# Kernel tuning notes

Hardware: AMD Instinct MI355X
Metric: run time of the kernel (lower is better)

Reference implementation:

```python
import jax, jax.numpy as jnp
import numpy as np

D_MODEL = 256

def setup_inputs() -> dict:
    key = jax.random.key(0)
    ks = jax.random.split(key, 6)
    B, Tx, Tm, D = 4, 512, 512, D_MODEL
    s = 1.0 / np.sqrt(D)
    return {
        "x": jax.random.normal(ks[0], (B, Tx, D), jnp.float32),
        "memory": jax.random.normal(ks[1], (B, Tm, D), jnp.float32),
        "memory_mask": jnp.ones((B, Tm), jnp.int32),
        "ws1_w": jax.random.uniform(ks[2], (D, D), jnp.float32, -s, s),
        "ws1_b": jax.random.uniform(ks[3], (D,), jnp.float32, -s, s),
        "ws2_w": jax.random.uniform(ks[4], (D, D), jnp.float32, -s, s),
        "wst_w": jax.random.uniform(ks[5], (D,), jnp.float32, -s, s),
    }

def reference(x, memory, memory_mask, ws1_w, ws1_b, ws2_w, wst_w):
    # item1: [B,Tx,D], item2: [B,Tm,D]  (torch Linear: y = x @ W^T + b)
    item1 = jnp.einsum("bxd,ed->bxe", x, ws1_w) + ws1_b
    item2 = jnp.einsum("bmd,ed->bme", memory, ws2_w)
    # broadcast add -> [B,Tx,Tm,D], tanh, reduce by wst -> scores [B,Tx,Tm]
    item = jnp.tanh(item1[:, :, None, :] + item2[:, None, :, :])
    S = jnp.einsum("bxmd,d->bxm", item, wst_w)
    S = jnp.where(memory_mask[:, None, :] == 0, -jnp.inf, S)
    S = jax.nn.softmax(S, axis=-1)
    out = jnp.einsum("bxm,bmd->bxd", S, memory)
    return (out, S)
```

## Files before the change

kernel.cpp:

```cpp
#include <hip/hip_runtime.h>

#define D_MODEL 256
#define TX 512
#define TM 512

__device__ __forceinline__ float fexp2(float x) { return __builtin_amdgcn_exp2f(x); }
__device__ __forceinline__ float frcp(float x)  { return __builtin_amdgcn_rcpf(x); }

__device__ __forceinline__ float quad(float4 a, float4 e, float4 w, float acc) {
    float p1 = fmaf(a.x, e.x, 1.f);
    float p2 = fmaf(a.y, e.y, 1.f);
    float p3 = fmaf(a.z, e.z, 1.f);
    float p4 = fmaf(a.w, e.w, 1.f);
    float p12 = p1 * p2;
    float p34 = p3 * p4;
    float q12 = fmaf(w.x, p2, w.y * p1);
    float q34 = fmaf(w.z, p4, w.w * p3);
    float N   = fmaf(q12, p34, q34 * p12);
    float D   = p12 * p34;
    return fmaf(N, frcp(D), acc);
}

__global__ __launch_bounds__(128) void gemm_exp2(
    const float* __restrict__ x,   const float* __restrict__ mem,
    const float* __restrict__ w1,  const float* __restrict__ b1,
    const float* __restrict__ w2,
    float* __restrict__ E1, float* __restrict__ E2p)
{
    const float C_SCALE = 2.8853900817779268f;
    const int bid = (int)blockIdx.x;
    const float* A; const float* W;
    int r0, n0;
    if (blockIdx.z == 0) { A = x;  W = w1; r0 = (bid & 63) * 32; n0 = (bid >> 6) * 64; }
    else                 { A = w2; W = mem; r0 = (bid & 7) * 32;  n0 = (bid >> 3) * 64; }

    __shared__ float As[2][16][36];
    __shared__ float Ws[2][16][68];
    const int tid = threadIdx.x;
    const int tx = tid & 15, ty = tid >> 4;
    const int rl = tid >> 2, g = tid & 3;
    float acc[4][4] = {};
    const float* Ap  = A + (size_t)(r0 + rl) * 256 + g * 4;
    const float* Wp0 = W + (size_t)(n0 + rl) * 256 + g * 4;
    const float* Wp1 = W + (size_t)(n0 + 32 + rl) * 256 + g * 4;

    {
        float4 a4 = *(const float4*)Ap;
        float4 w4 = *(const float4*)Wp0;
        float4 w5 = *(const float4*)Wp1;
        As[0][g*4+0][rl] = a4.x; As[0][g*4+1][rl] = a4.y;
        As[0][g*4+2][rl] = a4.z; As[0][g*4+3][rl] = a4.w;
        Ws[0][g*4+0][rl] = w4.x; Ws[0][g*4+1][rl] = w4.y;
        Ws[0][g*4+2][rl] = w4.z; Ws[0][g*4+3][rl] = w4.w;
        Ws[0][g*4+0][rl+32] = w5.x; Ws[0][g*4+1][rl+32] = w5.y;
        Ws[0][g*4+2][rl+32] = w5.z; Ws[0][g*4+3][rl+32] = w5.w;
    }
    __syncthreads();

    for (int k0 = 0; k0 < 16; ++k0) {
        const int cur = k0 & 1;
        float4 an, wn, vn;
        if (k0 < 15) {
            an = *(const float4*)(Ap  + (k0 + 1) * 16);
            wn = *(const float4*)(Wp0 + (k0 + 1) * 16);
            vn = *(const float4*)(Wp1 + (k0 + 1) * 16);
        }
        #pragma unroll
        for (int kk = 0; kk < 16; ++kk) {
            float4 av = *(const float4*)&As[cur][kk][ty*4];
            float4 wv = *(const float4*)&Ws[cur][kk][tx*4];
            float a_[4] = {av.x, av.y, av.z, av.w};
            float w_[4] = {wv.x, wv.y, wv.z, wv.w};
            #pragma unroll
            for (int i = 0; i < 4; ++i)
                #pragma unroll
                for (int j = 0; j < 4; ++j)
                    acc[i][j] = fmaf(a_[i], w_[j], acc[i][j]);
        }
        if (k0 < 15) {
            const int nxt = cur ^ 1;
            As[nxt][g*4+0][rl] = an.x; As[nxt][g*4+1][rl] = an.y;
            As[nxt][g*4+2][rl] = an.z; As[nxt][g*4+3][rl] = an.w;
            Ws[nxt][g*4+0][rl] = wn.x; Ws[nxt][g*4+1][rl] = wn.y;
            Ws[nxt][g*4+2][rl] = wn.z; Ws[nxt][g*4+3][rl] = wn.w;
            Ws[nxt][g*4+0][rl+32] = vn.x; Ws[nxt][g*4+1][rl+32] = vn.y;
            Ws[nxt][g*4+2][rl+32] = vn.z; Ws[nxt][g*4+3][rl+32] = vn.w;
            __syncthreads();
        }
    }

    if (blockIdx.z == 0) {
        #pragma unroll
        for (int i = 0; i < 4; ++i) {
            const int r = r0 + ty*4 + i;
            #pragma unroll
            for (int j = 0; j < 4; ++j) {
                const int n = n0 + tx*4 + j;
                E1[(size_t)r*256 + n] = fexp2(C_SCALE * (acc[i][j] + b1[n]));
            }
        }
    } else {
        #pragma unroll
        for (int i = 0; i < 4; ++i) {
            const int r = r0 + ty*4 + i;
            #pragma unroll
            for (int j = 0; j < 4; ++j) {
                const int n = n0 + tx*4 + j;
                E2p[(size_t)(r >> 2)*8192 + (size_t)n*4 + (r & 3)] = fexp2(C_SCALE * acc[i][j]);
            }
        }
    }
}

__global__ __launch_bounds__(512) void fused_tanh_attn(
    const float* __restrict__ E1,
    const float* __restrict__ E2p,
    const float* __restrict__ memory,
    const int*   __restrict__ mask,
    const float* __restrict__ wst,
    float* __restrict__ out,
    float* __restrict__ Sout)
{
    const float LOG2E = 1.4426950408889634f;
    const int t = threadIdx.x;
    const int blk = (int)((blockIdx.x & 7) * 64 + (blockIdx.x >> 3));
    const int b = blk >> 7;
    const int x0 = (blk & 127) * 4;
    const int wave = t >> 6, lane = t & 63;
    const int tm = t & 255;
    const int dh = t >> 8;

    __shared__ float i1R[4][D_MODEL];
    __shared__ float wsh[D_MODEL];
    __shared__ float P[4][TM];
    __shared__ float mneg[TM];
    __shared__ float opart[8][4][D_MODEL];
    __shared__ float wpart[8];
    __shared__ float smax[4][2], ssum[4][2];

    {
        const float* i1g = E1 + ((size_t)b * TX + x0) * D_MODEL;
        const int row = t >> 7, col2 = (t & 127) * 2;
        float2 v = *(const float2*)(i1g + (size_t)row * D_MODEL + col2);
        *(float2*)&i1R[row][col2] = v;
    }
    if (t < 256) wsh[t] = wst[t];
    mneg[t] = mask[b*TM + t] ? 0.f : -__builtin_inff();

    {
        float s = (t < 256) ? wst[t] : 0.f;
        #pragma unroll
        for (int off = 32; off > 0; off >>= 1) s += __shfl_xor(s, off);
        if (lane == 0) wpart[wave] = s;
    }

    const int g0 = dh * 32;
    const float* e2ptrA = E2p + ((size_t)b * TM + tm) * 4;
    const float* e2ptrB = e2ptrA + 1024;
    float4 e2a = *(const float4*)(e2ptrA + (size_t)g0 * 8192);
    float4 e2b = *(const float4*)(e2ptrB + (size_t)g0 * 8192);

    __syncthreads();
    const float Wsum = wpart[0] + wpart[1] + wpart[2] + wpart[3]
                     + wpart[4] + wpart[5] + wpart[6] + wpart[7];

    float accA[4] = {}, accB[4] = {};
    #pragma unroll 2
    for (int gi = 0; gi < 32; ++gi) {
        const int g = g0 + gi;
        float4 e2an = e2a, e2bn = e2b;
        if (gi < 31) {
            e2an = *(const float4*)(e2ptrA + (size_t)(g + 1) * 8192);
            e2bn = *(const float4*)(e2ptrB + (size_t)(g + 1) * 8192);
        }
        float4 w4 = *(const float4*)&wsh[g * 4];
        #pragma unroll
        for (int r = 0; r < 4; ++r) {
            float4 a = *(const float4*)&i1R[r][g * 4];
            accA[r] = quad(a, e2a, w4, accA[r]);
            accB[r] = quad(a, e2b, w4, accB[r]);
        }
        e2a = e2an; e2b = e2bn;
    }

    if (dh == 0) {
        #pragma unroll
        for (int r = 0; r < 4; ++r) {
            P[r][tm]       = accA[r];
            P[r][tm + 256] = accB[r];
        }
    }
    __syncthreads();
    if (dh == 1) {
        const float mnA = mneg[tm], mnB = mneg[tm + 256];
        #pragma unroll
        for (int r = 0; r < 4; ++r) {
            P[r][tm]       = Wsum - 2.f * (P[r][tm]       + accA[r]) + mnA;
            P[r][tm + 256] = Wsum - 2.f * (P[r][tm + 256] + accB[r]) + mnB;
        }
    }
    __syncthreads();

    {
        const int r = wave & 3, h = wave >> 2;
        const int base = h * 256 + lane * 4;
        float4 v4 = *(const float4*)&P[r][base];
        float v0 = v4.x, v1 = v4.y, v2 = v4.z, v3 = v4.w;
        float mx = fmaxf(fmaxf(v0, v1), fmaxf(v2, v3));
        #pragma unroll
        for (int off = 32; off > 0; off >>= 1) mx = fmaxf(mx, __shfl_xor(mx, off));
        float e0 = fexp2((v0 - mx) * LOG2E);
        float e1 = fexp2((v1 - mx) * LOG2E);
        float e2 = fexp2((v2 - mx) * LOG2E);
        float e3 = fexp2((v3 - mx) * LOG2E);
        float sum = (e0 + e1) + (e2 + e3);
        #pragma unroll
        for (int off = 32; off > 0; off >>= 1) sum += __shfl_xor(sum, off);
        if (lane == 0) { smax[r][h] = mx; ssum[r][h] = sum; }
        __syncthreads();
        const float m0 = smax[r][0], m1 = smax[r][1];
        const float mg = fmaxf(m0, m1);
        const float tot = ssum[r][0] * fexp2((m0 - mg) * LOG2E)
                        + ssum[r][1] * fexp2((m1 - mg) * LOG2E);
        const float fac = fexp2((mx - mg) * LOG2E) * frcp(tot);
        float4 p = {e0 * fac, e1 * fac, e2 * fac, e3 * fac};
        *(float4*)&P[r][base] = p;
        *(float4*)(Sout + ((size_t)b*TX + x0 + r) * TM + base) = p;
    }
    __syncthreads();

    {
        const int m0 = wave * 64;
        const float* memp = memory + ((size_t)b * TM + m0) * D_MODEL + lane * 4;
        float4 o0 = {0,0,0,0}, o1 = {0,0,0,0}, o2 = {0,0,0,0}, o3 = {0,0,0,0};
        for (int c = 0; c < 16; ++c) {
            float4 p0 = *(const float4*)&P[0][m0 + c*4];
            float4 p1 = *(const float4*)&P[1][m0 + c*4];
            float4 p2 = *(const float4*)&P[2][m0 + c*4];
            float4 p3 = *(const float4*)&P[3][m0 + c*4];
            #pragma unroll
            for (int j = 0; j < 4; ++j) {
                float4 mv = *(const float4*)(memp + (size_t)(c*4 + j) * D_MODEL);
                const float q0 = (j==0)?p0.x:(j==1)?p0.y:(j==2)?p0.z:p0.w;
                const float q1 = (j==0)?p1.x:(j==1)?p1.y:(j==2)?p1.z:p1.w;
                const float q2 = (j==0)?p2.x:(j==1)?p2.y:(j==2)?p2.z:p2.w;
                const float q3 = (j==0)?p3.x:(j==1)?p3.y:(j==2)?p3.z:p3.w;
                o0.x = fmaf(q0, mv.x, o0.x); o0.y = fmaf(q0, mv.y, o0.y);
                o0.z = fmaf(q0, mv.z, o0.z); o0.w = fmaf(q0, mv.w, o0.w);
                o1.x = fmaf(q1, mv.x, o1.x); o1.y = fmaf(q1, mv.y, o1.y);
                o1.z = fmaf(q1, mv.z, o1.z); o1.w = fmaf(q1, mv.w, o1.w);
                o2.x = fmaf(q2, mv.x, o2.x); o2.y = fmaf(q2, mv.y, o2.y);
                o2.z = fmaf(q2, mv.z, o2.z); o2.w = fmaf(q2, mv.w, o2.w);
                o3.x = fmaf(q3, mv.x, o3.x); o3.y = fmaf(q3, mv.y, o3.y);
                o3.z = fmaf(q3, mv.z, o3.z); o3.w = fmaf(q3, mv.w, o3.w);
            }
        }
        *(float4*)&opart[wave][0][lane*4] = o0;
        *(float4*)&opart[wave][1][lane*4] = o1;
        *(float4*)&opart[wave][2][lane*4] = o2;
        *(float4*)&opart[wave][3][lane*4] = o3;
    }
    __syncthreads();

    {
        #pragma unroll
        for (int k = 0; k < 2; ++k) {
            const int idx = t + k * 512;
            const int row = idx >> 8, d0 = idx & 255;
            float s = 0.f;
            #pragma unroll
            for (int w = 0; w < 8; ++w) s += opart[w][row][d0];
            out[((size_t)b*TX + x0 + row) * D_MODEL + d0] = s;
        }
    }
}

extern "C" void kernel_launch(void* const* d_in, const int* in_sizes, int n_in,
                              void* d_out, int out_size, void* d_ws, size_t ws_size,
                              hipStream_t stream) {
    const float* x    = (const float*)d_in[0];
    const float* mem  = (const float*)d_in[1];
    const int*   mask = (const int*)d_in[2];
    const float* w1   = (const float*)d_in[3];
    const float* b1   = (const float*)d_in[4];
    const float* w2   = (const float*)d_in[5];
    const float* wst  = (const float*)d_in[6];

    float* out  = (float*)d_out;
    float* Sout = out + 4 * 512 * 256;
    float* E1   = (float*)d_ws;
    float* E2p  = E1 + 4 * 512 * 256;

    dim3 gg(256, 1, 2);
    gemm_exp2<<<gg, 128, 0, stream>>>(x, mem, w1, b1, w2, E1, E2p);
    fused_tanh_attn<<<512, 512, 0, stream>>>(E1, E2p, mem, mask, wst, out, Sout);
}
```

Baseline: 58.90 us.

## Retile GEMM prologue to 64x64 tiles with 512-thread blocks

Rewrites the pre-GEMM kernel so each block computes a 64x64 output tile with 512 threads, each thread holding a 2x4 accumulator instead of 4x4. Half the threads load A and half load W, so each thread issues one global load per k-step. This gives more threads per block and fewer, larger blocks (256 instead of 512) to raise latency hiding and cut per-thread register use. In exchange, per-thread compute intensity drops and the grid has fewer blocks to fill the CUs.

```diff
diff --git a/kernel.cpp b/kernel.cpp
--- a/kernel.cpp
+++ b/kernel.cpp
@@ -21,7 +21,7 @@
     return fmaf(N, frcp(D), acc);
 }
 
-__global__ __launch_bounds__(128) void gemm_exp2(
+__global__ __launch_bounds__(512) void gemm_exp2(
     const float* __restrict__ x,   const float* __restrict__ mem,
     const float* __restrict__ w1,  const float* __restrict__ b1,
     const float* __restrict__ w2,
@@ -31,68 +31,58 @@
     const int bid = (int)blockIdx.x;
     const float* A; const float* W;
     int r0, n0;
-    if (blockIdx.z == 0) { A = x;  W = w1; r0 = (bid & 63) * 32; n0 = (bid >> 6) * 64; }
-    else                 { A = w2; W = mem; r0 = (bid & 7) * 32;  n0 = (bid >> 3) * 64; }
-
-    __shared__ float As[2][16][36];
+    if (blockIdx.z == 0) { A = x;  W = w1; r0 = (bid & 31) * 64; n0 = (bid >> 5) * 64; }
+    else                 { A = w2; W = mem; r0 = (bid >> 5) * 64; n0 = (bid & 31) * 64; }
+
+    __shared__ float As[2][16][68];
     __shared__ float Ws[2][16][68];
-    const int tid = threadIdx.x;
-    const int tx = tid & 15, ty = tid >> 4;
-    const int rl = tid >> 2, g = tid & 3;
-    float acc[4][4] = {};
-    const float* Ap  = A + (size_t)(r0 + rl) * 256 + g * 4;
-    const float* Wp0 = W + (size_t)(n0 + rl) * 256 + g * 4;
-    const float* Wp1 = W + (size_t)(n0 + 32 + rl) * 256 + g * 4;
-
-    {
-        float4 a4 = *(const float4*)Ap;
-        float4 w4 = *(const float4*)Wp0;
-        float4 w5 = *(const float4*)Wp1;
-        As[0][g*4+0][rl] = a4.x; As[0][g*4+1][rl] = a4.y;
-        As[0][g*4+2][rl] = a4.z; As[0][g*4+3][rl] = a4.w;
-        Ws[0][g*4+0][rl] = w4.x; Ws[0][g*4+1][rl] = w4.y;
-        Ws[0][g*4+2][rl] = w4.z; Ws[0][g*4+3][rl] = w4.w;
-        Ws[0][g*4+0][rl+32] = w5.x; Ws[0][g*4+1][rl+32] = w5.y;
-        Ws[0][g*4+2][rl+32] = w5.z; Ws[0][g*4+3][rl+32] = w5.w;
+    const int t = threadIdx.x;
+    const int tx = t & 15, ty = t >> 4;
+    const int half = t >> 8;
+    const int st = t & 255;
+    const int rl = st >> 2, g = st & 3;
+    float acc[2][4] = {};
+    const float* Sp = (half == 0 ? A + (size_t)(r0 + rl) * 256
+                                 : W + (size_t)(n0 + rl) * 256) + g * 4;
+
+    {
+        float4 v = *(const float4*)Sp;
+        float (*dst)[16][68] = (half == 0) ? &As[0] : &Ws[0];
+        (*dst)[g*4+0][rl] = v.x; (*dst)[g*4+1][rl] = v.y;
+        (*dst)[g*4+2][rl] = v.z; (*dst)[g*4+3][rl] = v.w;
     }
     __syncthreads();
 
     for (int k0 = 0; k0 < 16; ++k0) {
         const int cur = k0 & 1;
-        float4 an, wn, vn;
-        if (k0 < 15) {
-            an = *(const float4*)(Ap  + (k0 + 1) * 16);
-            wn = *(const float4*)(Wp0 + (k0 + 1) * 16);
-            vn = *(const float4*)(Wp1 + (k0 + 1) * 16);
-        }
+        float4 nv;
+        if (k0 < 15) nv = *(const float4*)(Sp + (k0 + 1) * 16);
         #pragma unroll
         for (int kk = 0; kk < 16; ++kk) {
-            float4 av = *(const float4*)&As[cur][kk][ty*4];
+            float2 av = *(const float2*)&As[cur][kk][ty*2];
             float4 wv = *(const float4*)&Ws[cur][kk][tx*4];
-            float a_[4] = {av.x, av.y, av.z, av.w};
-            float w_[4] = {wv.x, wv.y, wv.z, wv.w};
-            #pragma unroll
-            for (int i = 0; i < 4; ++i)
-                #pragma unroll
-                for (int j = 0; j < 4; ++j)
-                    acc[i][j] = fmaf(a_[i], w_[j], acc[i][j]);
+            acc[0][0] = fmaf(av.x, wv.x, acc[0][0]);
+            acc[0][1] = fmaf(av.x, wv.y, acc[0][1]);
+            acc[0][2] = fmaf(av.x, wv.z, acc[0][2]);
+            acc[0][3] = fmaf(av.x, wv.w, acc[0][3]);
+            acc[1][0] = fmaf(av.y, wv.x, acc[1][0]);
+            acc[1][1] = fmaf(av.y, wv.y, acc[1][1]);
+            acc[1][2] = fmaf(av.y, wv.z, acc[1][2]);
+            acc[1][3] = fmaf(av.y, wv.w, acc[1][3]);
         }
         if (k0 < 15) {
             const int nxt = cur ^ 1;
-            As[nxt][g*4+0][rl] = an.x; As[nxt][g*4+1][rl] = an.y;
-            As[nxt][g*4+2][rl] = an.z; As[nxt][g*4+3][rl] = an.w;
-            Ws[nxt][g*4+0][rl] = wn.x; Ws[nxt][g*4+1][rl] = wn.y;
-            Ws[nxt][g*4+2][rl] = wn.z; Ws[nxt][g*4+3][rl] = wn.w;
-            Ws[nxt][g*4+0][rl+32] = vn.x; Ws[nxt][g*4+1][rl+32] = vn.y;
-            Ws[nxt][g*4+2][rl+32] = vn.z; Ws[nxt][g*4+3][rl+32] = vn.w;
+            float (*dst)[16][68] = (half == 0) ? &As[nxt] : &Ws[nxt];
+            (*dst)[g*4+0][rl] = nv.x; (*dst)[g*4+1][rl] = nv.y;
+            (*dst)[g*4+2][rl] = nv.z; (*dst)[g*4+3][rl] = nv.w;
             __syncthreads();
         }
     }
 
     if (blockIdx.z == 0) {
         #pragma unroll
-        for (int i = 0; i < 4; ++i) {
-            const int r = r0 + ty*4 + i;
+        for (int i = 0; i < 2; ++i) {
+            const int r = r0 + ty*2 + i;
             #pragma unroll
             for (int j = 0; j < 4; ++j) {
                 const int n = n0 + tx*4 + j;
@@ -101,8 +91,8 @@
         }
     } else {
         #pragma unroll
-        for (int i = 0; i < 4; ++i) {
-            const int r = r0 + ty*4 + i;
+        for (int i = 0; i < 2; ++i) {
+            const int r = r0 + ty*2 + i;
             #pragma unroll
             for (int j = 0; j < 4; ++j) {
                 const int n = n0 + tx*4 + j;
@@ -291,7 +281,7 @@
     float* E1   = (float*)d_ws;
     float* E2p  = E1 + 4 * 512 * 256;
 
-    dim3 gg(256, 1, 2);
-    gemm_exp2<<<gg, 128, 0, stream>>>(x, mem, w1, b1, w2, E1, E2p);
+    dim3 gg(128, 1, 2);
+    gemm_exp2<<<gg, 512, 0, stream>>>(x, mem, w1, b1, w2, E1, E2p);
     fused_tanh_attn<<<512, 512, 0, stream>>>(E1, E2p, mem, mask, wst, out, Sout);
 }
```

Result: faster. 56.92 us (median of 2 runs) (-3.3%).
